# Performance work log

Measured on AMD Instinct MI355X. Metric: run time of the kernel, lower is better.

Reference implementation:

```python
import jax, jax.numpy as jnp
import numpy as np


def setup_inputs() -> dict:
    key = jax.random.key(0)
    ks = jax.random.split(key, 13)
    B, T, D, H, E, C, S = 256, 64, 512, 512, 256, 6624, 26
    s = 0.05
    return {
        "batch_H": jax.random.normal(ks[0], (B, T, D), jnp.float32),
        "text": jax.random.randint(ks[1], (B, S), 0, C, jnp.int64),
        "W_i2h": jax.random.normal(ks[2], (H, D), jnp.float32) * s,
        "W_h2h": jax.random.normal(ks[3], (H, H), jnp.float32) * s,
        "b_h2h": jax.random.normal(ks[4], (H,), jnp.float32) * s,
        "w_score": jax.random.normal(ks[5], (H,), jnp.float32) * s,
        "W_ih": jax.random.normal(ks[6], (4 * H, D + E), jnp.float32) * s,
        "W_hh": jax.random.normal(ks[7], (4 * H, H), jnp.float32) * s,
        "b_ih": jax.random.normal(ks[8], (4 * H,), jnp.float32) * s,
        "b_hh": jax.random.normal(ks[9], (4 * H,), jnp.float32) * s,
        "emb": jax.random.normal(ks[10], (C, E), jnp.float32) * s,
        "W_gen": jax.random.normal(ks[11], (C, H), jnp.float32) * s,
        "b_gen": jax.random.normal(ks[12], (C,), jnp.float32) * s,
        "max_label_length": 25,
    }


def reference(batch_H, text, W_i2h, W_h2h, b_h2h, w_score, W_ih, W_hh,
              b_ih, b_hh, emb, W_gen, b_gen, max_label_length):
    B, T, D = batch_H.shape
    H = W_h2h.shape[0]
    num_steps = max_label_length + 1

    # i2h(batch_H) is constant across steps -> hoist out of the recurrence
    Hproj = jnp.einsum('btd,hd->bth', batch_H, W_i2h)  # [B,T,H]
    char_embs = emb[text[:, :num_steps]]               # [B,S,E]
    xs = jnp.transpose(char_embs, (1, 0, 2))           # [S,B,E]

    def step(carry, ce):
        h, c = carry
        hp = h @ W_h2h.T + b_h2h                       # [B,H]
        e = jnp.tanh(Hproj + hp[:, None, :]) @ w_score  # [B,T]
        alpha = jax.nn.softmax(e, axis=1)
        context = jnp.einsum('bt,btd->bd', alpha, batch_H)  # [B,D]
        x = jnp.concatenate([context, ce], axis=1)     # [B,D+E]
        gates = x @ W_ih.T + b_ih + h @ W_hh.T + b_hh  # [B,4H]
        i, f, g, o = jnp.split(gates, 4, axis=1)
        c_new = jax.nn.sigmoid(f) * c + jax.nn.sigmoid(i) * jnp.tanh(g)
        h_new = jax.nn.sigmoid(o) * jnp.tanh(c_new)
        return (h_new, c_new), h_new

    h0 = jnp.zeros((B, H), batch_H.dtype)
    c0 = jnp.zeros((B, H), batch_H.dtype)
    _, hs = jax.lax.scan(step, (h0, c0), xs)           # hs: [S,B,H]
    output_hiddens = jnp.transpose(hs, (1, 0, 2))      # [B,S,H]
    probs = output_hiddens @ W_gen.T + b_gen           # [B,S,C]
    return probs
```

## Files before the change

### kernel.cpp

```cpp
#include <hip/hip_runtime.h>

typedef unsigned short u16;
typedef unsigned int   u32;
typedef __attribute__((ext_vector_type(4))) float f32x4;
typedef __attribute__((ext_vector_type(8))) u16   u16x8;
typedef __attribute__((ext_vector_type(4))) u16   u16x4;
typedef __attribute__((ext_vector_type(4))) u32   u32x4;

__device__ __forceinline__ u16 f2bf(float x) {
  u32 u = __builtin_bit_cast(u32, x);
  u = (u + 0x7fffu + ((u >> 16) & 1u)) >> 16;
  return (u16)u;
}
__device__ __forceinline__ float bf2f(u16 h) {
  return __builtin_bit_cast(float, (u32)h << 16);
}
__device__ __forceinline__ float fast_sig(float x) { return 1.f / (1.f + __expf(-x)); }
__device__ __forceinline__ float fast_tanh(float x) {
  float e = __expf(2.f * x);
  return 1.f - 2.f / (e + 1.f);
}

__device__ __forceinline__ f32x4 mfma_bf16(u16x8 a, u16x8 b, f32x4 c) {
  asm volatile("v_mfma_f32_16x16x32_bf16 %0, %1, %2, %0" : "+v"(c) : "v"(a), "v"(b));
  return c;
}

__device__ __forceinline__ void gload_lds16(const void* g, void* l) {
  __builtin_amdgcn_global_load_lds(
      (__attribute__((address_space(1))) u32*)g,
      (__attribute__((address_space(3))) u32*)l, 16, 0, 0);
}

__device__ __forceinline__ void conv4(const float* __restrict__ s, u16* __restrict__ d, int i) {
  f32x4 v = *(const f32x4*)(s + i);
  u16x4 o;
  o.x = f2bf(v.x); o.y = f2bf(v.y); o.z = f2bf(v.z); o.w = f2bf(v.w);
  *(u16x4*)(d + i) = o;
}

__global__ __launch_bounds__(256) void k_prep(
    const float* __restrict__ batch_H, const float* __restrict__ W_i2h,
    const float* __restrict__ emb, const float* __restrict__ W_ih,
    const float* __restrict__ W_h2h, const float* __restrict__ W_hh,
    const float* __restrict__ W_gen, const float* __restrict__ b_ih,
    const float* __restrict__ b_hh, const float* __restrict__ b_h2h,
    u16* __restrict__ bHb, u16* __restrict__ Wi2hb, u16* __restrict__ embb,
    u16* __restrict__ Wctxb, u16* __restrict__ Wceb, u16* __restrict__ Whcatb,
    u16* __restrict__ Wgenb, float* __restrict__ biascat,
    u16* __restrict__ hb, float* __restrict__ cst,
    float* __restrict__ hpbuf, float* __restrict__ ghbuf) {
  const u32 u = blockIdx.x * 256 + threadIdx.x;
  if (u < 2097152u) { conv4(batch_H, bHb, u * 4); return; }
  if (u < 2162688u) { conv4(W_i2h, Wi2hb, (u - 2097152u) * 4); return; }
  if (u < 2586624u) { conv4(emb, embb, (u - 2162688u) * 4); return; }
  if (u < 2588672u) {
    *(u16x4*)(embb + 1695744u + (u - 2586624u) * 4) = (u16x4){0, 0, 0, 0};
    return;
  }
  if (u < 2850816u) {
    int i = (u - 2588672u) * 4;
    int r = i >> 9, c = i & 511;
    f32x4 v = *(const f32x4*)(W_ih + (size_t)r * 768 + c);
    u16x4 o;
    o.x = f2bf(v.x); o.y = f2bf(v.y); o.z = f2bf(v.z); o.w = f2bf(v.w);
    *(u16x4*)(Wctxb + i) = o;
    return;
  }
  if (u < 2981888u) {
    int i = (u - 2850816u) * 4;
    int r = i >> 8, c = i & 255;
    f32x4 v = *(const f32x4*)(W_ih + (size_t)r * 768 + 512 + c);
    u16x4 o;
    o.x = f2bf(v.x); o.y = f2bf(v.y); o.z = f2bf(v.z); o.w = f2bf(v.w);
    *(u16x4*)(Wceb + i) = o;
    return;
  }
  if (u < 3309568u) {
    int i = (u - 2981888u) * 4;
    int r = i >> 9, c = i & 511;
    const float* src = (r < 512) ? (W_h2h + (size_t)r * 512 + c)
                                 : (W_hh + (size_t)(r - 512) * 512 + c);
    f32x4 v = *(const f32x4*)src;
    u16x4 o;
    o.x = f2bf(v.x); o.y = f2bf(v.y); o.z = f2bf(v.z); o.w = f2bf(v.w);
    *(u16x4*)(Whcatb + i) = o;
    return;
  }
  if (u < 4161536u) {
    int i = (u - 3309568u) * 4;
    int r = i >> 9;
    if (r < 6624) conv4(W_gen, Wgenb, i);
    else *(u16x4*)(Wgenb + i) = (u16x4){0, 0, 0, 0};
    return;
  }
  if (u < 4162048u) {
    int j = (u - 4161536u) * 4;
    f32x4 a = *(const f32x4*)(b_ih + j), b = *(const f32x4*)(b_hh + j);
    f32x4 r = {a.x + b.x, a.y + b.y, a.z + b.z, a.w + b.w};
    *(f32x4*)(biascat + j) = r;
    return;
  }
  if (u < 4178432u) {
    *(u32x4*)((char*)hb + (size_t)(u - 4162048u) * 16) = (u32x4){0, 0, 0, 0};
    return;
  }
  if (u < 4211200u) {
    *(u32x4*)((char*)cst + (size_t)(u - 4178432u) * 16) = (u32x4){0, 0, 0, 0};
    return;
  }
  if (u < 4243968u) {
    int i = (u - 4211200u) * 4;
    int j = i & 511;
    *(f32x4*)(hpbuf + i) = *(const f32x4*)(b_h2h + j);
    return;
  }
  if (u < 4375040u) {
    *(u32x4*)((char*)ghbuf + (size_t)(u - 4243968u) * 16) = (u32x4){0, 0, 0, 0};
    return;
  }
}

template <int OUT_MODE>
__device__ __forceinline__ void gemm128_body(
    const u16* __restrict__ A, int lda, const u16* __restrict__ B, int ldb,
    const float* __restrict__ bias, float* __restrict__ Cf, u16* __restrict__ Cb,
    int ldc, int Nreal, int K, int m0, int n0, char* smem) {
  u16* sA = (u16*)smem;
  u16* sB = (u16*)(smem + 32768);
  const int tid = threadIdx.x;
  const int lane = tid & 63, wave = tid >> 6;
  const int wr = wave >> 1, wc = wave & 1;
  const int l15 = lane & 15, lhi = lane >> 4;

  f32x4 acc[4][4];
#pragma unroll
  for (int i = 0; i < 4; ++i)
#pragma unroll
    for (int j = 0; j < 4; ++j) acc[i][j] = 0.f;

  for (int k0 = 0; k0 < K; k0 += 128) {
    __syncthreads();
#pragma unroll
    for (int j = 0; j < 8; ++j) {
      int idx = j * 256 + tid, row = idx >> 4, cc = idx & 15, c = cc ^ (row & 15);
      gload_lds16(A + (size_t)(m0 + row) * lda + (k0 + c * 8), sA + idx * 8);
    }
#pragma unroll
    for (int j = 0; j < 8; ++j) {
      int idx = j * 256 + tid, row = idx >> 4, cc = idx & 15, c = cc ^ (row & 15);
      gload_lds16(B + (size_t)(n0 + row) * ldb + (k0 + c * 8), sB + idx * 8);
    }
    __syncthreads();

#pragma unroll
    for (int ks = 0; ks < 4; ++ks) {
      u16x8 av[4], bv[4];
#pragma unroll
      for (int mi = 0; mi < 4; ++mi) {
        int row = wr * 64 + mi * 16 + l15;
        int ch = row * 16 + ((ks * 4 + lhi) ^ (row & 15));
        av[mi] = *(const u16x8*)(sA + ch * 8);
      }
#pragma unroll
      for (int ni = 0; ni < 4; ++ni) {
        int row = wc * 64 + ni * 16 + l15;
        int ch = row * 16 + ((ks * 4 + lhi) ^ (row & 15));
        bv[ni] = *(const u16x8*)(sB + ch * 8);
      }
#pragma unroll
      for (int mi = 0; mi < 4; ++mi)
#pragma unroll
        for (int ni = 0; ni < 4; ++ni) acc[mi][ni] = mfma_bf16(av[mi], bv[ni], acc[mi][ni]);
    }
  }

  asm volatile("s_nop 7\ns_nop 7\ns_nop 7");

#pragma unroll
  for (int mi = 0; mi < 4; ++mi) {
#pragma unroll
    for (int ni = 0; ni < 4; ++ni) {
      int col = n0 + wc * 64 + ni * 16 + l15;
      if (col < Nreal) {
        float bvv = (OUT_MODE == 1) ? bias[col] : 0.f;
#pragma unroll
        for (int r = 0; r < 4; ++r) {
          int row = m0 + wr * 64 + mi * 16 + lhi * 4 + r;
          float v = acc[mi][ni][r] + bvv;
          if (OUT_MODE == 2)
            Cb[(size_t)row * ldc + col] = f2bf(v);
          else
            Cf[(size_t)row * ldc + col] = v;
        }
      }
    }
  }
}

template <int OUT_MODE, bool SWZ>
__global__ __launch_bounds__(256) void kGemm128(const u16* __restrict__ A, int lda,
                                                const u16* __restrict__ B, int ldb,
                                                const float* __restrict__ bias,
                                                float* __restrict__ Cf, u16* __restrict__ Cb,
                                                int ldc, int Nreal, int K) {
  __shared__ __align__(16) char smem[65536];
  int bx = blockIdx.x, by = blockIdx.y;
  if (SWZ) {
    int gx = gridDim.x;
    int lin = by * gx + bx;
    int q = (gx * gridDim.y) >> 3;
    int idx = (lin & 7) * q + (lin >> 3);
    by = idx / gx;
    bx = idx - by * gx;
  }
  gemm128_body<OUT_MODE>(A, lda, B, ldb, bias, Cf, Cb, ldc, Nreal, K,
                         by * 128, bx * 128, smem);
}

__global__ __launch_bounds__(256) void kHE(const u16* __restrict__ bHb,
                                           const u16* __restrict__ Wi2hb,
                                           u16* __restrict__ Hproj,
                                           const u16* __restrict__ embb,
                                           const u16* __restrict__ Wceb,
                                           const float* __restrict__ biascat,
                                           float* __restrict__ E2G) {
  __shared__ __align__(16) char smem[65536];
  const int bid = blockIdx.x;
  if (bid < 512) {
    gemm128_body<2>(bHb, 512, Wi2hb, 512, nullptr, nullptr, Hproj, 512, 512, 512,
                    (bid >> 2) * 128, (bid & 3) * 128, smem);
  } else {
    int r = bid - 512;
    gemm128_body<1>(embb, 256, Wceb, 256, biascat, E2G, nullptr, 2048, 2048, 256,
                    (r >> 4) * 128, (r & 15) * 128, smem);
  }
}

__global__ __launch_bounds__(256) void kA_hpgh(const u16* __restrict__ hb,
                                               const u16* __restrict__ Whcatb,
                                               const float* __restrict__ b_h2h,
                                               float* __restrict__ hpbuf,
                                               float* __restrict__ ghbuf) {
  extern __shared__ __align__(16) char smem[];
  u16* sA = (u16*)smem;
  u16* sB = (u16*)(smem + 32768);
  const int tid = threadIdx.x;
  const int lane = tid & 63, wave = tid >> 6;
  const int wr = wave >> 1, wc = wave & 1;
  const int l15 = lane & 15, lhi = lane >> 4;
  const int b0 = ((int)blockIdx.x / 20) * 32, n0 = ((int)blockIdx.x % 20) * 128;

#pragma unroll
  for (int j = 0; j < 8; ++j) {
    int idx = j * 256 + tid, row = idx >> 6, cc = idx & 63, c = cc ^ (row & 15);
    gload_lds16(hb + (size_t)(b0 + row) * 512 + c * 8, sA + idx * 8);
  }
#pragma unroll
  for (int j = 0; j < 32; ++j) {
    int idx = j * 256 + tid, row = idx >> 6, cc = idx & 63, c = cc ^ (row & 15);
    gload_lds16(Whcatb + (size_t)(n0 + row) * 512 + c * 8, sB + idx * 8);
  }
  __syncthreads();

  f32x4 acc[4];
#pragma unroll
  for (int j = 0; j < 4; ++j) acc[j] = 0.f;
#pragma unroll
  for (int ks = 0; ks < 16; ++ks) {
    u16x8 av, bv[4];
    {
      int row = wr * 16 + l15;
      int ch = row * 64 + ((ks * 4 + lhi) ^ (row & 15));
      av = *(const u16x8*)(sA + ch * 8);
    }
#pragma unroll
    for (int ni = 0; ni < 4; ++ni) {
      int row = wc * 64 + ni * 16 + l15;
      int ch = row * 64 + ((ks * 4 + lhi) ^ (row & 15));
      bv[ni] = *(const u16x8*)(sB + ch * 8);
    }
#pragma unroll
    for (int ni = 0; ni < 4; ++ni) acc[ni] = mfma_bf16(av, bv[ni], acc[ni]);
  }
  asm volatile("s_nop 7\ns_nop 7\ns_nop 7");
#pragma unroll
  for (int ni = 0; ni < 4; ++ni) {
    int col = n0 + wc * 64 + ni * 16 + l15;
    int rowg = b0 + wr * 16 + lhi * 4;
    if (col < 512) {
      float bvv = b_h2h[col];
#pragma unroll
      for (int r = 0; r < 4; ++r)
        hpbuf[(size_t)(rowg + r) * 512 + col] = acc[ni][r] + bvv;
    } else {
#pragma unroll
      for (int r = 0; r < 4; ++r)
        ghbuf[(size_t)(rowg + r) * 2048 + col - 512] = acc[ni][r];
    }
  }
}

__global__ __launch_bounds__(256) void kB_attn(const u16* __restrict__ Hproj,
                                               const float* __restrict__ hpbuf,
                                               const float* __restrict__ wsc,
                                               const u16* __restrict__ bh,
                                               u16* __restrict__ ctxb) {
  const int b = blockIdx.x, tid = threadIdx.x;
  __shared__ float hpsp[528];
  __shared__ float wssp[528];
  __shared__ float es[64];

  {
    int j0 = tid * 2;
    hpsp[j0 + (j0 >> 5)] = hpbuf[(size_t)b * 512 + j0];
    hpsp[j0 + 1 + ((j0 + 1) >> 5)] = hpbuf[(size_t)b * 512 + j0 + 1];
    int pi = j0 + (j0 >> 5);
    wssp[pi] = wsc[j0];
    wssp[pi + 1] = wsc[j0 + 1];
  }
  __syncthreads();

  const int ch16 = tid & 15;
  const int hbase = ch16 * 33;
  const int hc = ch16 * 32;
  float hpr[32], wsr[32];
#pragma unroll
  for (int j = 0; j < 32; ++j) {
    hpr[j] = hpsp[hbase + j];
    wsr[j] = wssp[hbase + j];
  }
#pragma unroll
  for (int tg = 0; tg < 4; ++tg) {
    int t = tg * 16 + (tid >> 4);
    const u16* hr = Hproj + (size_t)(b * 64 + t) * 512 + hc;
    float s = 0.f;
#pragma unroll
    for (int jo = 0; jo < 32; jo += 8) {
      u16x8 hv = *(const u16x8*)(hr + jo);
#pragma unroll
      for (int j = 0; j < 8; ++j) {
        float x = bf2f(hv[j]) + hpr[jo + j];
        s += fast_tanh(x) * wsr[jo + j];
      }
    }
#pragma unroll
    for (int off = 8; off; off >>= 1) s += __shfl_xor(s, off, 16);
    if (ch16 == 0) es[t] = s;
  }
  __syncthreads();
  if (tid < 64) {
    float v = es[tid];
    float m = v;
#pragma unroll
    for (int o = 32; o; o >>= 1) m = fmaxf(m, __shfl_xor(m, o, 64));
    float p = __expf(v - m);
    float su = p;
#pragma unroll
    for (int o = 32; o; o >>= 1) su += __shfl_xor(su, o, 64);
    es[tid] = p / su;
  }
  __syncthreads();
  const u16* base = bh + (size_t)b * 32768 + tid * 2;
  float c0 = 0.f, c1 = 0.f;
#pragma unroll 8
  for (int t = 0; t < 64; ++t) {
    u32 w = *(const u32*)(base + t * 512);
    float a = es[t];
    c0 = fmaf(a, bf2f((u16)(w & 0xffffu)), c0);
    c1 = fmaf(a, bf2f((u16)(w >> 16)), c1);
  }
  u32 pk = (u32)f2bf(c0) | ((u32)f2bf(c1) << 16);
  *(u32*)(ctxb + (size_t)b * 512 + tid * 2) = pk;
}

__global__ __launch_bounds__(256) void kC_gates_lstm(const u16* __restrict__ ctxb,
                                                     const u16* __restrict__ Wctxb,
                                                     const float* __restrict__ E2G,
                                                     const float* __restrict__ ghbuf,
                                                     const int* __restrict__ text,
                                                     float* __restrict__ cst,
                                                     u16* __restrict__ hb,
                                                     u16* __restrict__ hsb, int step) {
  extern __shared__ __align__(16) char smem[];
  u16* sA = (u16*)smem;
  u16* sB = (u16*)(smem + 32768);
  const int tid = threadIdx.x;
  const int lane = tid & 63, wave = tid >> 6;
  const int wr = wave >> 1, wc = wave & 1;
  const int l15 = lane & 15, lhi = lane >> 4;
  const int jt = blockIdx.x;
  const int b0 = blockIdx.y * 32;

#pragma unroll
  for (int j = 0; j < 8; ++j) {
    int idx = j * 256 + tid, row = idx >> 6, cc = idx & 63, c = cc ^ (row & 15);
    gload_lds16(ctxb + (size_t)(b0 + row) * 512 + c * 8, sA + idx * 8);
  }
#pragma unroll
  for (int j = 0; j < 32; ++j) {
    int idx = j * 256 + tid, row = idx >> 6, cc = idx & 63, c = cc ^ (row & 15);
    int grow = (row >> 5) * 512 + jt * 32 + (row & 31);
    gload_lds16(Wctxb + (size_t)grow * 512 + c * 8, sB + idx * 8);
  }
  __syncthreads();

  f32x4 acc[4];
#pragma unroll
  for (int j = 0; j < 4; ++j) acc[j] = 0.f;
#pragma unroll
  for (int ks = 0; ks < 16; ++ks) {
    u16x8 av, bv[4];
    {
      int row = wr * 16 + l15;
      int ch = row * 64 + ((ks * 4 + lhi) ^ (row & 15));
      av = *(const u16x8*)(sA + ch * 8);
    }
#pragma unroll
    for (int ni = 0; ni < 4; ++ni) {
      int row = wc * 64 + ni * 16 + l15;
      int ch = row * 64 + ((ks * 4 + lhi) ^ (row & 15));
      bv[ni] = *(const u16x8*)(sB + ch * 8);
    }
#pragma unroll
    for (int ni = 0; ni < 4; ++ni) acc[ni] = mfma_bf16(av, bv[ni], acc[ni]);
  }

  asm volatile("s_nop 7\ns_nop 7\ns_nop 7");
  __syncthreads();
  float (*gsm)[132] = (float(*)[132])smem;
#pragma unroll
  for (int ni = 0; ni < 4; ++ni) {
    int col = wc * 64 + ni * 16 + l15;
    int row = wr * 16 + lhi * 4;
#pragma unroll
    for (int r = 0; r < 4; ++r) gsm[row + r][col] = acc[ni][r];
  }
  __syncthreads();

  {
    const int bl = tid >> 3, jl0 = (tid & 7) * 4;
    const int b = b0 + bl;
    const int jg0 = jt * 32 + jl0;
    const int ci = text[b * 26 + step];
    const float* gh = ghbuf + (size_t)b * 2048;
    const float* ge = E2G + (size_t)ci * 2048;
    float cn[4];
    u16 hbv[4];
#pragma unroll
    for (int q = 0; q < 4; ++q) {
      int jl = jl0 + q, j = jg0 + q;
      float gi = gsm[bl][jl]      + gh[j]        + ge[j];
      float gf = gsm[bl][32 + jl] + gh[512 + j]  + ge[512 + j];
      float gg = gsm[bl][64 + jl] + gh[1024 + j] + ge[1024 + j];
      float go = gsm[bl][96 + jl] + gh[1536 + j] + ge[1536 + j];
      float c = fast_sig(gf) * cst[(size_t)b * 512 + j] + fast_sig(gi) * fast_tanh(gg);
      cn[q] = c;
      hbv[q] = f2bf(fast_sig(go) * fast_tanh(c));
    }
    *(f32x4*)(cst + (size_t)b * 512 + jg0) = *(f32x4*)cn;
    *(u16x4*)(hb + (size_t)b * 512 + jg0) = *(u16x4*)hbv;
    *(u16x4*)(hsb + (size_t)(b * 26 + step) * 512 + jg0) = *(u16x4*)hbv;
  }
}

extern "C" void kernel_launch(void* const* d_in, const int* in_sizes, int n_in,
                              void* d_out, int out_size, void* d_ws, size_t ws_size,
                              hipStream_t stream) {
  const float* batch_H = (const float*)d_in[0];
  const int*   text    = (const int*)d_in[1];
  const float* W_i2h   = (const float*)d_in[2];
  const float* W_h2h   = (const float*)d_in[3];
  const float* b_h2h   = (const float*)d_in[4];
  const float* w_score = (const float*)d_in[5];
  const float* W_ih    = (const float*)d_in[6];
  const float* W_hh    = (const float*)d_in[7];
  const float* b_ih    = (const float*)d_in[8];
  const float* b_hh    = (const float*)d_in[9];
  const float* emb     = (const float*)d_in[10];
  const float* W_gen   = (const float*)d_in[11];
  const float* b_gen   = (const float*)d_in[12];
  float* out = (float*)d_out;

  static bool attr_done = []() {
    hipFuncSetAttribute(reinterpret_cast<const void*>(kA_hpgh),
                        hipFuncAttributeMaxDynamicSharedMemorySize, 163840);
    hipFuncSetAttribute(reinterpret_cast<const void*>(kC_gates_lstm),
                        hipFuncAttributeMaxDynamicSharedMemorySize, 163840);
    return true;
  }();
  (void)attr_done;

  u16* bHb   = (u16*)d_out;
  u16* Hproj = bHb + 8388608;

  char* w = (char*)d_ws;
  auto alloc = [&](size_t bytes) {
    char* p = w;
    w += (bytes + 255) & ~(size_t)255;
    return p;
  };
  u16*   Wi2hb   = (u16*)alloc(512ull * 512 * 2);
  u16*   Whcatb  = (u16*)alloc(2560ull * 512 * 2);
  u16*   Wctxb   = (u16*)alloc(2048ull * 512 * 2);
  u16*   Wceb    = (u16*)alloc(2048ull * 256 * 2);
  u16*   Wgenb   = (u16*)alloc(6656ull * 512 * 2);
  u16*   embb    = (u16*)alloc(6656ull * 256 * 2);
  float* biascat = (float*)alloc(2048ull * 4);
  u16*   ctxb    = (u16*)alloc(256ull * 512 * 2);
  u16*   hb      = (u16*)alloc(256ull * 512 * 2);
  float* cst     = (float*)alloc(256ull * 512 * 4);
  float* hpbuf   = (float*)alloc(256ull * 512 * 4);
  float* ghbuf   = (float*)alloc(256ull * 2048 * 4);
  u16*   hsb     = (u16*)alloc(6656ull * 512 * 2);
  float* E2G     = (float*)alloc(6656ull * 2048 * 4);

  k_prep<<<17090, 256, 0, stream>>>(batch_H, W_i2h, emb, W_ih, W_h2h, W_hh, W_gen,
                                    b_ih, b_hh, b_h2h, bHb, Wi2hb, embb, Wctxb, Wceb,
                                    Whcatb, Wgenb, biascat, hb, cst, hpbuf, ghbuf);

  kHE<<<1344, 256, 0, stream>>>(bHb, Wi2hb, Hproj, embb, Wceb, biascat, E2G);

  for (int s = 0; s < 26; ++s) {
    if (s > 0)
      kA_hpgh<<<160, 256, 163840, stream>>>(hb, Whcatb, b_h2h, hpbuf, ghbuf);
    kB_attn<<<256, 256, 0, stream>>>(Hproj, hpbuf, w_score, bHb, ctxb);
    kC_gates_lstm<<<dim3(16, 8), 256, 163840, stream>>>(ctxb, Wctxb, E2G, ghbuf, text,
                                                        cst, hb, hsb, s);
  }

  kGemm128<1, true><<<dim3(52, 52), 256, 0, stream>>>(
      hsb, 512, Wgenb, 512, b_gen, out, nullptr, 6624, 6624, 512);

  (void)in_sizes; (void)n_in; (void)out_size; (void)ws_size;
}
```

Baseline: 780.7 us.

## Store E2G table in bf16 and retile recurrent step kernels for more blocks

The precomputed embedding-to-gate table is now written and read in bf16 instead of fp32, which halves its footprint and the gather traffic in each LSTM step. The h-projection kernel changes its tile from 32x128 to 64x64 per block. The gates kernel now covers 16 hidden units per block instead of 32, which doubles the grid to 256 blocks and cuts shared memory per block. The aim is to raise parallelism in the latency-bound per-step kernels. The cost is slight precision loss in the gate bias table and more redundant loading of the A operand across blocks.

```diff
diff --git a/kernel.cpp b/kernel.cpp
--- a/kernel.cpp
+++ b/kernel.cpp
@@ -2,6 +2,7 @@
 
 typedef unsigned short u16;
 typedef unsigned int   u32;
+typedef __attribute__((ext_vector_type(2))) float f32x2;
 typedef __attribute__((ext_vector_type(4))) float f32x4;
 typedef __attribute__((ext_vector_type(8))) u16   u16x8;
 typedef __attribute__((ext_vector_type(4))) u16   u16x4;
@@ -183,12 +184,12 @@
     for (int ni = 0; ni < 4; ++ni) {
       int col = n0 + wc * 64 + ni * 16 + l15;
       if (col < Nreal) {
-        float bvv = (OUT_MODE == 1) ? bias[col] : 0.f;
+        float bvv = (OUT_MODE == 1 || OUT_MODE == 3) ? bias[col] : 0.f;
 #pragma unroll
         for (int r = 0; r < 4; ++r) {
           int row = m0 + wr * 64 + mi * 16 + lhi * 4 + r;
           float v = acc[mi][ni][r] + bvv;
-          if (OUT_MODE == 2)
+          if (OUT_MODE == 2 || OUT_MODE == 3)
             Cb[(size_t)row * ldc + col] = f2bf(v);
           else
             Cf[(size_t)row * ldc + col] = v;
@@ -224,7 +225,7 @@
                                            const u16* __restrict__ embb,
                                            const u16* __restrict__ Wceb,
                                            const float* __restrict__ biascat,
-                                           float* __restrict__ E2G) {
+                                           u16* __restrict__ E2Gb) {
   __shared__ __align__(16) char smem[65536];
   const int bid = blockIdx.x;
   if (bid < 512) {
@@ -232,7 +233,7 @@
                     (bid >> 2) * 128, (bid & 3) * 128, smem);
   } else {
     int r = bid - 512;
-    gemm128_body<1>(embb, 256, Wceb, 256, biascat, E2G, nullptr, 2048, 2048, 256,
+    gemm128_body<3>(embb, 256, Wceb, 256, biascat, nullptr, E2Gb, 2048, 2048, 256,
                     (r >> 4) * 128, (r & 15) * 128, smem);
   }
 }
@@ -244,20 +245,19 @@
                                                float* __restrict__ ghbuf) {
   extern __shared__ __align__(16) char smem[];
   u16* sA = (u16*)smem;
-  u16* sB = (u16*)(smem + 32768);
+  u16* sB = (u16*)(smem + 65536);
   const int tid = threadIdx.x;
   const int lane = tid & 63, wave = tid >> 6;
-  const int wr = wave >> 1, wc = wave & 1;
   const int l15 = lane & 15, lhi = lane >> 4;
-  const int b0 = ((int)blockIdx.x / 20) * 32, n0 = ((int)blockIdx.x % 20) * 128;
-
-#pragma unroll
-  for (int j = 0; j < 8; ++j) {
+  const int b0 = ((int)blockIdx.x / 40) * 64, n0 = ((int)blockIdx.x % 40) * 64;
+
+#pragma unroll
+  for (int j = 0; j < 16; ++j) {
     int idx = j * 256 + tid, row = idx >> 6, cc = idx & 63, c = cc ^ (row & 15);
     gload_lds16(hb + (size_t)(b0 + row) * 512 + c * 8, sA + idx * 8);
   }
 #pragma unroll
-  for (int j = 0; j < 32; ++j) {
+  for (int j = 0; j < 16; ++j) {
     int idx = j * 256 + tid, row = idx >> 6, cc = idx & 63, c = cc ^ (row & 15);
     gload_lds16(Whcatb + (size_t)(n0 + row) * 512 + c * 8, sB + idx * 8);
   }
@@ -270,13 +270,13 @@
   for (int ks = 0; ks < 16; ++ks) {
     u16x8 av, bv[4];
     {
-      int row = wr * 16 + l15;
+      int row = wave * 16 + l15;
       int ch = row * 64 + ((ks * 4 + lhi) ^ (row & 15));
       av = *(const u16x8*)(sA + ch * 8);
     }
 #pragma unroll
     for (int ni = 0; ni < 4; ++ni) {
-      int row = wc * 64 + ni * 16 + l15;
+      int row = ni * 16 + l15;
       int ch = row * 64 + ((ks * 4 + lhi) ^ (row & 15));
       bv[ni] = *(const u16x8*)(sB + ch * 8);
     }
@@ -286,8 +286,8 @@
   asm volatile("s_nop 7\ns_nop 7\ns_nop 7");
 #pragma unroll
   for (int ni = 0; ni < 4; ++ni) {
-    int col = n0 + wc * 64 + ni * 16 + l15;
-    int rowg = b0 + wr * 16 + lhi * 4;
+    int col = n0 + ni * 16 + l15;
+    int rowg = b0 + wave * 16 + lhi * 4;
     if (col < 512) {
       float bvv = b_h2h[col];
 #pragma unroll
@@ -376,7 +376,7 @@
 
 __global__ __launch_bounds__(256) void kC_gates_lstm(const u16* __restrict__ ctxb,
                                                      const u16* __restrict__ Wctxb,
-                                                     const float* __restrict__ E2G,
+                                                     const u16* __restrict__ E2Gb,
                                                      const float* __restrict__ ghbuf,
                                                      const int* __restrict__ text,
                                                      float* __restrict__ cst,
@@ -389,7 +389,7 @@
   const int lane = tid & 63, wave = tid >> 6;
   const int wr = wave >> 1, wc = wave & 1;
   const int l15 = lane & 15, lhi = lane >> 4;
-  const int jt = blockIdx.x;
+  const int jj = blockIdx.x;
   const int b0 = blockIdx.y * 32;
 
 #pragma unroll
@@ -398,40 +398,40 @@
     gload_lds16(ctxb + (size_t)(b0 + row) * 512 + c * 8, sA + idx * 8);
   }
 #pragma unroll
-  for (int j = 0; j < 32; ++j) {
+  for (int j = 0; j < 16; ++j) {
     int idx = j * 256 + tid, row = idx >> 6, cc = idx & 63, c = cc ^ (row & 15);
-    int grow = (row >> 5) * 512 + jt * 32 + (row & 31);
+    int grow = (row >> 4) * 512 + jj * 16 + (row & 15);
     gload_lds16(Wctxb + (size_t)grow * 512 + c * 8, sB + idx * 8);
   }
   __syncthreads();
 
-  f32x4 acc[4];
-#pragma unroll
-  for (int j = 0; j < 4; ++j) acc[j] = 0.f;
+  f32x4 acc[2];
+#pragma unroll
+  for (int j = 0; j < 2; ++j) acc[j] = 0.f;
 #pragma unroll
   for (int ks = 0; ks < 16; ++ks) {
-    u16x8 av, bv[4];
+    u16x8 av, bv[2];
     {
       int row = wr * 16 + l15;
       int ch = row * 64 + ((ks * 4 + lhi) ^ (row & 15));
       av = *(const u16x8*)(sA + ch * 8);
     }
 #pragma unroll
-    for (int ni = 0; ni < 4; ++ni) {
-      int row = wc * 64 + ni * 16 + l15;
+    for (int ni = 0; ni < 2; ++ni) {
+      int row = wc * 32 + ni * 16 + l15;
       int ch = row * 64 + ((ks * 4 + lhi) ^ (row & 15));
       bv[ni] = *(const u16x8*)(sB + ch * 8);
     }
 #pragma unroll
-    for (int ni = 0; ni < 4; ++ni) acc[ni] = mfma_bf16(av, bv[ni], acc[ni]);
+    for (int ni = 0; ni < 2; ++ni) acc[ni] = mfma_bf16(av, bv[ni], acc[ni]);
   }
 
   asm volatile("s_nop 7\ns_nop 7\ns_nop 7");
   __syncthreads();
-  float (*gsm)[132] = (float(*)[132])smem;
-#pragma unroll
-  for (int ni = 0; ni < 4; ++ni) {
-    int col = wc * 64 + ni * 16 + l15;
+  float (*gsm)[68] = (float(*)[68])smem;
+#pragma unroll
+  for (int ni = 0; ni < 2; ++ni) {
+    int col = wc * 32 + ni * 16 + l15;
     int row = wr * 16 + lhi * 4;
 #pragma unroll
     for (int r = 0; r < 4; ++r) gsm[row + r][col] = acc[ni][r];
@@ -439,28 +439,29 @@
   __syncthreads();
 
   {
-    const int bl = tid >> 3, jl0 = (tid & 7) * 4;
+    const int bl = tid >> 3, jl = (tid & 7) * 2;
     const int b = b0 + bl;
-    const int jg0 = jt * 32 + jl0;
+    const int jg = jj * 16 + jl;
     const int ci = text[b * 26 + step];
     const float* gh = ghbuf + (size_t)b * 2048;
-    const float* ge = E2G + (size_t)ci * 2048;
-    float cn[4];
-    u16 hbv[4];
-#pragma unroll
-    for (int q = 0; q < 4; ++q) {
-      int jl = jl0 + q, j = jg0 + q;
-      float gi = gsm[bl][jl]      + gh[j]        + ge[j];
-      float gf = gsm[bl][32 + jl] + gh[512 + j]  + ge[512 + j];
-      float gg = gsm[bl][64 + jl] + gh[1024 + j] + ge[1024 + j];
-      float go = gsm[bl][96 + jl] + gh[1536 + j] + ge[1536 + j];
+    const u16* ge = E2Gb + (size_t)ci * 2048;
+    float cn[2];
+    u16 hbv[2];
+#pragma unroll
+    for (int q = 0; q < 2; ++q) {
+      int jc = jl + q, j = jg + q;
+      float gi = gsm[bl][jc]      + gh[j]        + bf2f(ge[j]);
+      float gf = gsm[bl][16 + jc] + gh[512 + j]  + bf2f(ge[512 + j]);
+      float gg = gsm[bl][32 + jc] + gh[1024 + j] + bf2f(ge[1024 + j]);
+      float go = gsm[bl][48 + jc] + gh[1536 + j] + bf2f(ge[1536 + j]);
       float c = fast_sig(gf) * cst[(size_t)b * 512 + j] + fast_sig(gi) * fast_tanh(gg);
       cn[q] = c;
       hbv[q] = f2bf(fast_sig(go) * fast_tanh(c));
     }
-    *(f32x4*)(cst + (size_t)b * 512 + jg0) = *(f32x4*)cn;
-    *(u16x4*)(hb + (size_t)b * 512 + jg0) = *(u16x4*)hbv;
-    *(u16x4*)(hsb + (size_t)(b * 26 + step) * 512 + jg0) = *(u16x4*)hbv;
+    *(f32x2*)(cst + (size_t)b * 512 + jg) = *(f32x2*)cn;
+    u32 pk = (u32)hbv[0] | ((u32)hbv[1] << 16);
+    *(u32*)(hb + (size_t)b * 512 + jg) = pk;
+    *(u32*)(hsb + (size_t)(b * 26 + step) * 512 + jg) = pk;
   }
 }
 
@@ -513,20 +514,20 @@
   float* hpbuf   = (float*)alloc(256ull * 512 * 4);
   float* ghbuf   = (float*)alloc(256ull * 2048 * 4);
   u16*   hsb     = (u16*)alloc(6656ull * 512 * 2);
-  float* E2G     = (float*)alloc(6656ull * 2048 * 4);
+  u16*   E2Gb    = (u16*)alloc(6656ull * 2048 * 2);
 
   k_prep<<<17090, 256, 0, stream>>>(batch_H, W_i2h, emb, W_ih, W_h2h, W_hh, W_gen,
                                     b_ih, b_hh, b_h2h, bHb, Wi2hb, embb, Wctxb, Wceb,
                                     Whcatb, Wgenb, biascat, hb, cst, hpbuf, ghbuf);
 
-  kHE<<<1344, 256, 0, stream>>>(bHb, Wi2hb, Hproj, embb, Wceb, biascat, E2G);
+  kHE<<<1344, 256, 0, stream>>>(bHb, Wi2hb, Hproj, embb, Wceb, biascat, E2Gb);
 
   for (int s = 0; s < 26; ++s) {
     if (s > 0)
-      kA_hpgh<<<160, 256, 163840, stream>>>(hb, Whcatb, b_h2h, hpbuf, ghbuf);
+      kA_hpgh<<<160, 256, 131072, stream>>>(hb, Whcatb, b_h2h, hpbuf, ghbuf);
     kB_attn<<<256, 256, 0, stream>>>(Hproj, hpbuf, w_score, bHb, ctxb);
-    kC_gates_lstm<<<dim3(16, 8), 256, 163840, stream>>>(ctxb, Wctxb, E2G, ghbuf, text,
-                                                        cst, hb, hsb, s);
+    kC_gates_lstm<<<dim3(32, 8), 256, 98304, stream>>>(ctxb, Wctxb, E2Gb, ghbuf, text,
+                                                       cst, hb, hsb, s);
   }
 
   kGemm128<1, true><<<dim3(52, 52), 256, 0, stream>>>(
```

Result: no change. 766.1 us, median of 2 (-1.9%).
